# Kernel tuning notes

Measured on AMD Instinct MI355X. Metric: run time of the kernel, lower is better.

The kernel has to match this reference:

```python
import jax, jax.numpy as jnp
import numpy as np

N_NODES = 500000


def _gcn_conv(x, W, b, src, dst, n):
    # x: [N, Fin], W: [Fin, Fout]. PyG GCNConv with add_self_loops + sym norm.
    h = x @ W                                            # [N, Fout]
    deg = jax.ops.segment_sum(jnp.ones_like(dst, dtype=h.dtype), dst,
                              num_segments=n)            # in-degree incl self loops
    dinv = jnp.where(deg > 0, jax.lax.rsqrt(jnp.maximum(deg, 1)), 0.0)
    norm = dinv[src] * dinv[dst]                         # [E]
    msg = h[src] * norm[:, None]                         # gather + scale
    out = jax.ops.segment_sum(msg, dst, num_segments=n)  # scatter-add to targets
    return out + b


def setup_inputs() -> dict:
    key = jax.random.key(0)
    k1, k2, k3, k4 = jax.random.split(key, 4)
    x = jax.random.normal(k1, (N_NODES, 1), dtype=jnp.float32)
    edge_index = jax.random.randint(k2, (2, 8000000), 0, N_NODES, dtype=jnp.int64)
    W1 = jax.random.normal(k3, (1, 32), dtype=jnp.float32) * (1.0 / np.sqrt(1))
    b1 = jnp.zeros((32,), dtype=jnp.float32)
    W2 = jax.random.normal(k4, (32, 2), dtype=jnp.float32) * (1.0 / np.sqrt(32))
    b2 = jnp.zeros((2,), dtype=jnp.float32)
    return {"x": x, "edge_index": edge_index, "W1": W1, "b1": b1, "W2": W2, "b2": b2}


def reference(x, edge_index, W1, b1, W2, b2):
    n = x.shape[0]
    loops = jnp.arange(n, dtype=edge_index.dtype)
    src = jnp.concatenate([edge_index[0], loops])  # add self-loops
    dst = jnp.concatenate([edge_index[1], loops])
    h = _gcn_conv(x, W1, b1, src, dst, n)
    h = jax.nn.relu(h)
    # F.dropout(training=self.training): identity in eval mode
    h = _gcn_conv(h, W2, b2, src, dst, n)
    return jax.nn.log_softmax(h, axis=1)
```

## Files before the change

### kernel.cpp

```cpp
#include <hip/hip_runtime.h>


static constexpr int BKT_BITS = 11;
static constexpr int BKT = 1 << BKT_BITS;
static constexpr int NB = 256;
static constexpr int HB = 512;
static constexpr int HT = 256;
static constexpr int CHUNK = 8192;
static constexpr int SCT = 256;
static constexpr int PERT = CHUNK / SCT;
static constexpr int CLS_SH = 27;
static constexpr int NCLS = 8;
static constexpr int NW = 16;

using u32x4 = __attribute__((ext_vector_type(4))) unsigned;

__global__ void __launch_bounds__(HT) k_hist(const int* __restrict__ dst, int e,
                                             int chunk, int nbkt,
                                             unsigned* __restrict__ totals) {
  __shared__ unsigned cnt[NB];
  for (int t = threadIdx.x; t < NB; t += HT) cnt[t] = 0;
  __syncthreads();
  int lo = blockIdx.x * chunk;
  int hi = min(lo + chunk, e);
  const int4* d4 = (const int4*)dst;
  for (int i = (lo >> 2) + threadIdx.x; i < (hi >> 2); i += HT) {
    int4 d = d4[i];
    atomicAdd(&cnt[((unsigned)d.x) >> BKT_BITS], 1u);
    atomicAdd(&cnt[((unsigned)d.y) >> BKT_BITS], 1u);
    atomicAdd(&cnt[((unsigned)d.z) >> BKT_BITS], 1u);
    atomicAdd(&cnt[((unsigned)d.w) >> BKT_BITS], 1u);
  }
  for (int i = ((hi >> 2) << 2) + threadIdx.x; i < hi; i += HT)
    atomicAdd(&cnt[((unsigned)dst[i]) >> BKT_BITS], 1u);
  __syncthreads();
  for (int t = threadIdx.x; t < nbkt; t += HT)
    if (cnt[t]) atomicAdd(&totals[t], cnt[t]);
}

__global__ void k_basescan(const unsigned* __restrict__ totals, int nbkt,
                           unsigned* __restrict__ gcur) {
  int lane = threadIdx.x;
  unsigned running = 0;
  for (int c = 0; c < NB; c += 64) {
    int k = c + lane;
    unsigned v = (k < nbkt) ? totals[k] : 0u;
    unsigned incl = v;
#pragma unroll
    for (int off = 1; off < 64; off <<= 1) {
      unsigned t = __shfl_up(incl, off);
      if (lane >= off) incl += t;
    }
    if (k < nbkt) gcur[k] = running + incl - v;
    running += __shfl(incl, 63);
  }
}

__global__ void __launch_bounds__(SCT) k_scatter(
    const int* __restrict__ src, const int* __restrict__ dst, int e, int nbkt,
    unsigned* __restrict__ gcur, unsigned* __restrict__ packed) {
  __shared__ unsigned staged[CHUNK];
  __shared__ unsigned cnt[NB];
  __shared__ unsigned cur[NB];
  __shared__ unsigned gseg[NB];
  __shared__ unsigned loff[NB + 1];
  const int tid = threadIdx.x;
  const int lo = blockIdx.x * CHUNK;
  for (int t = tid; t < NB; t += SCT) { cnt[t] = 0u; cur[t] = 0u; }
  __syncthreads();

  unsigned pk[PERT];
  unsigned bku[PERT / 4];
  const int4* s4 = (const int4*)src;
  const int4* d4 = (const int4*)dst;
#pragma unroll
  for (int jj = 0; jj < PERT / 4; ++jj) {
    int i4 = (lo >> 2) + jj * SCT + tid;
    unsigned b4 = 0xFFFFFFFFu;
    if (i4 * 4 + 3 < e) {
      int4 s = s4[i4];
      int4 d = d4[i4];
      unsigned k0 = ((unsigned)d.x) >> BKT_BITS, k1 = ((unsigned)d.y) >> BKT_BITS;
      unsigned k2 = ((unsigned)d.z) >> BKT_BITS, k3 = ((unsigned)d.w) >> BKT_BITS;
      pk[jj * 4 + 0] = ((unsigned)s.x << BKT_BITS) | ((unsigned)d.x & (BKT - 1));
      pk[jj * 4 + 1] = ((unsigned)s.y << BKT_BITS) | ((unsigned)d.y & (BKT - 1));
      pk[jj * 4 + 2] = ((unsigned)s.z << BKT_BITS) | ((unsigned)d.z & (BKT - 1));
      pk[jj * 4 + 3] = ((unsigned)s.w << BKT_BITS) | ((unsigned)d.w & (BKT - 1));
      b4 = k0 | (k1 << 8) | (k2 << 16) | (k3 << 24);
      atomicAdd(&cnt[k0], 1u);
      atomicAdd(&cnt[k1], 1u);
      atomicAdd(&cnt[k2], 1u);
      atomicAdd(&cnt[k3], 1u);
    } else {
#pragma unroll
      for (int c = 0; c < 4; ++c) {
        int i = i4 * 4 + c;
        if (i >= lo && i < e) {
          unsigned dd = (unsigned)dst[i];
          unsigned kk = dd >> BKT_BITS;
          pk[jj * 4 + c] = ((unsigned)src[i] << BKT_BITS) | (dd & (BKT - 1));
          b4 = (b4 & ~(0xFFu << (8 * c))) | (kk << (8 * c));
          atomicAdd(&cnt[kk], 1u);
        }
      }
    }
    bku[jj] = b4;
  }
  __syncthreads();

  if (tid < 64) {
    unsigned running = 0;
    for (int c = 0; c < NB; c += 64) {
      int k = c + tid;
      unsigned v = cnt[k];
      unsigned incl = v;
#pragma unroll
      for (int off = 1; off < 64; off <<= 1) {
        unsigned t = __shfl_up(incl, off);
        if (tid >= off) incl += t;
      }
      loff[k] = running + incl - v;
      running += __shfl(incl, 63);
    }
    if (tid == 0) loff[NB] = running;
  }
  __syncthreads();

  for (int k = tid; k < nbkt; k += SCT)
    if (cnt[k]) gseg[k] = atomicAdd(&gcur[k], cnt[k]);

#pragma unroll
  for (int jj = 0; jj < PERT / 4; ++jj) {
    unsigned b4 = bku[jj];
#pragma unroll
    for (int c = 0; c < 4; ++c) {
      unsigned k = (b4 >> (8 * c)) & 0xFFu;
      if (k != 0xFFu) {
        unsigned pos = loff[k] + atomicAdd(&cur[k], 1u);
        staged[pos] = pk[jj * 4 + c];
      }
    }
  }
  __syncthreads();

  int mv = (int)loff[NB];
  for (int t = tid; t < mv; t += SCT) {
    int a = 0, b = nbkt;
    while (b - a > 1) {
      int mid = (a + b) >> 1;
      if ((int)loff[mid] <= t) a = mid; else b = mid;
    }
    __builtin_nontemporal_store(staged[t],
                                packed + gseg[a] + (unsigned)(t - (int)loff[a]));
  }
}

__global__ void __launch_bounds__(1024) k_classort(
    const unsigned* __restrict__ packed, const unsigned* __restrict__ gcur,
    const float* __restrict__ x, int n, unsigned* __restrict__ packed2,
    float* __restrict__ dinv, float* __restrict__ xs) {
  __shared__ unsigned cnt_node[BKT];
  __shared__ unsigned wcnt[NCLS * NW];
  __shared__ unsigned wcur[NCLS * NW];
  const int k = blockIdx.x;
  const int tid = threadIdx.x;
  const int w = tid >> 6;
  for (int t = tid; t < BKT; t += 1024) cnt_node[t] = 0;
  if (tid < NCLS * NW) wcnt[tid] = 0;
  __syncthreads();
  unsigned lo = k ? gcur[k - 1] : 0u, hi = gcur[k];
  unsigned loA = (lo + 3u) & ~3u, hiA = hi & ~3u;
  if (loA > hi) loA = hi;
  if (hiA < loA) hiA = loA;

  for (unsigned i = lo + tid; i < loA; i += 1024) {
    unsigned p = packed[i];
    atomicAdd(&cnt_node[p & (BKT - 1)], 1u);
    atomicAdd(&wcnt[(p >> CLS_SH) * NW + w], 1u);
  }
  for (unsigned i = hiA + tid; i < hi; i += 1024) {
    unsigned p = packed[i];
    atomicAdd(&cnt_node[p & (BKT - 1)], 1u);
    atomicAdd(&wcnt[(p >> CLS_SH) * NW + w], 1u);
  }
  const u32x4* p4 = (const u32x4*)packed;
  for (unsigned q = (loA >> 2) + tid; q < (hiA >> 2); q += 1024) {
    u32x4 p = p4[q];
    atomicAdd(&cnt_node[p.x & (BKT - 1)], 1u);
    atomicAdd(&wcnt[(p.x >> CLS_SH) * NW + w], 1u);
    atomicAdd(&cnt_node[p.y & (BKT - 1)], 1u);
    atomicAdd(&wcnt[(p.y >> CLS_SH) * NW + w], 1u);
    atomicAdd(&cnt_node[p.z & (BKT - 1)], 1u);
    atomicAdd(&wcnt[(p.z >> CLS_SH) * NW + w], 1u);
    atomicAdd(&cnt_node[p.w & (BKT - 1)], 1u);
    atomicAdd(&wcnt[(p.w >> CLS_SH) * NW + w], 1u);
  }
  __syncthreads();

  if (tid < 64) {
    unsigned running = 0;
#pragma unroll
    for (int r = 0; r < (NCLS * NW) / 64; ++r) {
      int idx = r * 64 + tid;
      unsigned v = wcnt[idx];
      unsigned incl = v;
#pragma unroll
      for (int off = 1; off < 64; off <<= 1) {
        unsigned t = __shfl_up(incl, off);
        if (tid >= off) incl += t;
      }
      wcur[idx] = running + incl - v;
      running += __shfl(incl, 63);
    }
  }
  __syncthreads();

  for (unsigned i = lo + tid; i < loA; i += 1024) {
    unsigned p = packed[i];
    unsigned pos = atomicAdd(&wcur[(p >> CLS_SH) * NW + w], 1u);
    packed2[lo + pos] = p;
  }
  for (unsigned i = hiA + tid; i < hi; i += 1024) {
    unsigned p = packed[i];
    unsigned pos = atomicAdd(&wcur[(p >> CLS_SH) * NW + w], 1u);
    packed2[lo + pos] = p;
  }
  for (unsigned q = (loA >> 2) + tid; q < (hiA >> 2); q += 1024) {
    u32x4 p = p4[q];
    unsigned pos0 = atomicAdd(&wcur[(p.x >> CLS_SH) * NW + w], 1u);
    packed2[lo + pos0] = p.x;
    unsigned pos1 = atomicAdd(&wcur[(p.y >> CLS_SH) * NW + w], 1u);
    packed2[lo + pos1] = p.y;
    unsigned pos2 = atomicAdd(&wcur[(p.z >> CLS_SH) * NW + w], 1u);
    packed2[lo + pos2] = p.z;
    unsigned pos3 = atomicAdd(&wcur[(p.w >> CLS_SH) * NW + w], 1u);
    packed2[lo + pos3] = p.w;
  }

  int g0 = k << BKT_BITS;
  for (int t = tid; t < BKT; t += 1024) {
    int g = g0 + t;
    if (g < n) {
      float di = rsqrtf((float)(cnt_node[t] + 1u));
      dinv[g] = di;
      xs[g] = di * x[g];
    }
  }
}

__global__ void __launch_bounds__(1024) k_accA2(
    const unsigned* __restrict__ packed2, const unsigned* __restrict__ gcur,
    const float* __restrict__ dinv, const float* __restrict__ xs,
    const float* __restrict__ W1, const float* __restrict__ b1,
    const float* __restrict__ W2, int n, float2* __restrict__ yd) {
  __shared__ float acc[BKT];
  __shared__ float sW1[32], sb1[32], sW2[64];
  if (threadIdx.x < 32) {
    sW1[threadIdx.x] = W1[threadIdx.x];
    sb1[threadIdx.x] = b1[threadIdx.x];
  } else if (threadIdx.x < 96) {
    sW2[threadIdx.x - 32] = W2[threadIdx.x - 32];
  }
  for (int t = threadIdx.x; t < BKT; t += 1024) acc[t] = 0.0f;
  __syncthreads();
  int k = blockIdx.x;
  unsigned lo = k ? gcur[k - 1] : 0u, hi = gcur[k];
  unsigned loA = (lo + 3u) & ~3u, hiA = hi & ~3u;
  if (loA > hi) loA = hi;
  if (hiA < loA) hiA = loA;
  for (unsigned i = lo + threadIdx.x; i < loA; i += 1024) {
    unsigned p = packed2[i];
    atomicAdd(&acc[p & (BKT - 1)], xs[p >> BKT_BITS]);
  }
  for (unsigned i = hiA + threadIdx.x; i < hi; i += 1024) {
    unsigned p = packed2[i];
    atomicAdd(&acc[p & (BKT - 1)], xs[p >> BKT_BITS]);
  }
  const u32x4* p4 = (const u32x4*)packed2;
  for (unsigned q = (loA >> 2) + threadIdx.x; q < (hiA >> 2); q += 1024) {
    u32x4 p = __builtin_nontemporal_load(p4 + q);
    float v0 = xs[p.x >> BKT_BITS];
    float v1 = xs[p.y >> BKT_BITS];
    float v2 = xs[p.z >> BKT_BITS];
    float v3 = xs[p.w >> BKT_BITS];
    atomicAdd(&acc[p.x & (BKT - 1)], v0);
    atomicAdd(&acc[p.y & (BKT - 1)], v1);
    atomicAdd(&acc[p.z & (BKT - 1)], v2);
    atomicAdd(&acc[p.w & (BKT - 1)], v3);
  }
  __syncthreads();
  int g0 = k << BKT_BITS;
  for (int t = threadIdx.x; t < BKT; t += 1024) {
    int g = g0 + t;
    if (g >= n) continue;
    float di = dinv[g];
    float s = di * (acc[t] + xs[g]);
    float y0 = 0.0f, y1 = 0.0f;
#pragma unroll
    for (int f = 0; f < 32; ++f) {
      float h = fmaxf(fmaf(s, sW1[f], sb1[f]), 0.0f);
      y0 = fmaf(h, sW2[2 * f + 0], y0);
      y1 = fmaf(h, sW2[2 * f + 1], y1);
    }
    yd[g] = make_float2(di * y0, di * y1);
  }
}

__global__ void __launch_bounds__(1024) k_accB3(
    const unsigned* __restrict__ packed2, const unsigned* __restrict__ gcur,
    const float* __restrict__ dinv, const float2* __restrict__ yd,
    const float* __restrict__ b2, int n, float2* __restrict__ out) {
  __shared__ float a0[BKT], a1[BKT];
  for (int t = threadIdx.x; t < BKT; t += 1024) {
    a0[t] = 0.0f;
    a1[t] = 0.0f;
  }
  __syncthreads();
  int k = blockIdx.x;
  unsigned lo = k ? gcur[k - 1] : 0u, hi = gcur[k];
  unsigned loA = (lo + 3u) & ~3u, hiA = hi & ~3u;
  if (loA > hi) loA = hi;
  if (hiA < loA) hiA = loA;
  for (unsigned i = lo + threadIdx.x; i < loA; i += 1024) {
    unsigned p = packed2[i];
    float2 v = yd[p >> BKT_BITS];
    atomicAdd(&a0[p & (BKT - 1)], v.x);
    atomicAdd(&a1[p & (BKT - 1)], v.y);
  }
  for (unsigned i = hiA + threadIdx.x; i < hi; i += 1024) {
    unsigned p = packed2[i];
    float2 v = yd[p >> BKT_BITS];
    atomicAdd(&a0[p & (BKT - 1)], v.x);
    atomicAdd(&a1[p & (BKT - 1)], v.y);
  }
  const u32x4* p4 = (const u32x4*)packed2;
  for (unsigned q = (loA >> 2) + threadIdx.x; q < (hiA >> 2); q += 1024) {
    u32x4 p = __builtin_nontemporal_load(p4 + q);
    float2 v0 = yd[p.x >> BKT_BITS];
    float2 v1 = yd[p.y >> BKT_BITS];
    float2 v2 = yd[p.z >> BKT_BITS];
    float2 v3 = yd[p.w >> BKT_BITS];
    atomicAdd(&a0[p.x & (BKT - 1)], v0.x);
    atomicAdd(&a1[p.x & (BKT - 1)], v0.y);
    atomicAdd(&a0[p.y & (BKT - 1)], v1.x);
    atomicAdd(&a1[p.y & (BKT - 1)], v1.y);
    atomicAdd(&a0[p.z & (BKT - 1)], v2.x);
    atomicAdd(&a1[p.z & (BKT - 1)], v2.y);
    atomicAdd(&a0[p.w & (BKT - 1)], v3.x);
    atomicAdd(&a1[p.w & (BKT - 1)], v3.y);
  }
  __syncthreads();
  float b20 = b2[0], b21 = b2[1];
  int g0 = k << BKT_BITS;
  for (int t = threadIdx.x; t < BKT; t += 1024) {
    int g = g0 + t;
    if (g >= n) continue;
    float di = dinv[g];
    float2 yv = yd[g];
    float t0 = fmaf(di, a0[t] + yv.x, b20);
    float t1 = fmaf(di, a1[t] + yv.y, b21);
    float m = fmaxf(t0, t1);
    float l = m + logf(expf(t0 - m) + expf(t1 - m));
    out[g] = make_float2(t0 - l, t1 - l);
  }
}

extern "C" void kernel_launch(void* const* d_in, const int* in_sizes, int n_in,
                              void* d_out, int out_size, void* d_ws, size_t ws_size,
                              hipStream_t stream) {
  const float* x = (const float*)d_in[0];
  const int* edge = (const int*)d_in[1];
  const float* W1 = (const float*)d_in[2];
  const float* b1 = (const float*)d_in[3];
  const float* W2 = (const float*)d_in[4];
  const float* b2 = (const float*)d_in[5];
  float2* out = (float2*)d_out;

  const int n = in_sizes[0];
  const int e = in_sizes[1] / 2;
  const int* src = edge;
  const int* dst = edge + e;

  const int nbkt = (n + BKT - 1) >> BKT_BITS;
  const int hchunk = (((e + HB - 1) / HB) + 3) & ~3;
  const int sgrid = (e + CHUNK - 1) / CHUNK;

  char* ws = (char*)d_ws;
  size_t off = 0;
  unsigned* packed = (unsigned*)(ws + off);  off += (size_t)e * 4;
  unsigned* packed2 = (unsigned*)(ws + off); off += (size_t)e * 4;
  unsigned* totals = (unsigned*)(ws + off);  off += NB * 4;
  unsigned* gcur = (unsigned*)(ws + off);    off += NB * 4;
  float* dinv = (float*)(ws + off);          off += (size_t)n * 4;
  float* xs = (float*)(ws + off);            off += (size_t)n * 4;
  float2* yd = (float2*)(ws + off);          off += (size_t)n * 8;

  hipMemsetAsync(totals, 0, NB * sizeof(unsigned), stream);
  k_hist<<<HB, HT, 0, stream>>>(dst, e, hchunk, nbkt, totals);
  k_basescan<<<1, 64, 0, stream>>>(totals, nbkt, gcur);
  k_scatter<<<sgrid, SCT, 0, stream>>>(src, dst, e, nbkt, gcur, packed);
  k_classort<<<nbkt, 1024, 0, stream>>>(packed, gcur, x, n, packed2, dinv, xs);
  k_accA2<<<nbkt, 1024, 0, stream>>>(packed2, gcur, dinv, xs, W1, b1, W2, n, yd);
  k_accB3<<<nbkt, 1024, 0, stream>>>(packed2, gcur, dinv, yd, b2, n, out);
}
```

Baseline: 253.9 us.

## Tile edge aggregation by source slice with LDS-staged features and two-way partials

```diff
diff --git a/kernel.cpp b/kernel.cpp
--- a/kernel.cpp
+++ b/kernel.cpp
@@ -9,8 +9,8 @@
 static constexpr int CHUNK = 8192;
 static constexpr int SCT = 256;
 static constexpr int PERT = CHUNK / SCT;
-static constexpr int CLS_SH = 27;
-static constexpr int NCLS = 8;
+static constexpr int NCLS = 245;
+static constexpr int NCLSP = 248;
 static constexpr int NW = 16;
 
 using u32x4 = __attribute__((ext_vector_type(4))) unsigned;
@@ -158,15 +158,16 @@
 __global__ void __launch_bounds__(1024) k_classort(
     const unsigned* __restrict__ packed, const unsigned* __restrict__ gcur,
     const float* __restrict__ x, int n, unsigned* __restrict__ packed2,
-    float* __restrict__ dinv, float* __restrict__ xs) {
+    unsigned* __restrict__ sliceoff, unsigned short* __restrict__ deg16,
+    float* __restrict__ xs) {
   __shared__ unsigned cnt_node[BKT];
-  __shared__ unsigned wcnt[NCLS * NW];
-  __shared__ unsigned wcur[NCLS * NW];
+  __shared__ unsigned wcnt[NCLSP * NW];
+  __shared__ unsigned wcur[NCLSP * NW];
   const int k = blockIdx.x;
   const int tid = threadIdx.x;
   const int w = tid >> 6;
   for (int t = tid; t < BKT; t += 1024) cnt_node[t] = 0;
-  if (tid < NCLS * NW) wcnt[tid] = 0;
+  for (int t = tid; t < NCLSP * NW; t += 1024) wcnt[t] = 0;
   __syncthreads();
   unsigned lo = k ? gcur[k - 1] : 0u, hi = gcur[k];
   unsigned loA = (lo + 3u) & ~3u, hiA = hi & ~3u;
@@ -176,32 +177,31 @@
   for (unsigned i = lo + tid; i < loA; i += 1024) {
     unsigned p = packed[i];
     atomicAdd(&cnt_node[p & (BKT - 1)], 1u);
-    atomicAdd(&wcnt[(p >> CLS_SH) * NW + w], 1u);
+    atomicAdd(&wcnt[(p >> 22) * NW + w], 1u);
   }
   for (unsigned i = hiA + tid; i < hi; i += 1024) {
     unsigned p = packed[i];
     atomicAdd(&cnt_node[p & (BKT - 1)], 1u);
-    atomicAdd(&wcnt[(p >> CLS_SH) * NW + w], 1u);
+    atomicAdd(&wcnt[(p >> 22) * NW + w], 1u);
   }
   const u32x4* p4 = (const u32x4*)packed;
   for (unsigned q = (loA >> 2) + tid; q < (hiA >> 2); q += 1024) {
     u32x4 p = p4[q];
     atomicAdd(&cnt_node[p.x & (BKT - 1)], 1u);
-    atomicAdd(&wcnt[(p.x >> CLS_SH) * NW + w], 1u);
+    atomicAdd(&wcnt[(p.x >> 22) * NW + w], 1u);
     atomicAdd(&cnt_node[p.y & (BKT - 1)], 1u);
-    atomicAdd(&wcnt[(p.y >> CLS_SH) * NW + w], 1u);
+    atomicAdd(&wcnt[(p.y >> 22) * NW + w], 1u);
     atomicAdd(&cnt_node[p.z & (BKT - 1)], 1u);
-    atomicAdd(&wcnt[(p.z >> CLS_SH) * NW + w], 1u);
+    atomicAdd(&wcnt[(p.z >> 22) * NW + w], 1u);
     atomicAdd(&cnt_node[p.w & (BKT - 1)], 1u);
-    atomicAdd(&wcnt[(p.w >> CLS_SH) * NW + w], 1u);
+    atomicAdd(&wcnt[(p.w >> 22) * NW + w], 1u);
   }
   __syncthreads();
 
   if (tid < 64) {
     unsigned running = 0;
-#pragma unroll
-    for (int r = 0; r < (NCLS * NW) / 64; ++r) {
-      int idx = r * 64 + tid;
+    for (int c = 0; c < NCLSP * NW; c += 64) {
+      int idx = c + tid;
       unsigned v = wcnt[idx];
       unsigned incl = v;
 #pragma unroll
@@ -209,7 +209,10 @@
         unsigned t = __shfl_up(incl, off);
         if (tid >= off) incl += t;
       }
-      wcur[idx] = running + incl - v;
+      unsigned excl = running + incl - v;
+      wcur[idx] = excl;
+      if ((idx & (NW - 1)) == 0 && (idx >> 4) <= NCLS)
+        sliceoff[k * (NCLS + 1) + (idx >> 4)] = excl;
       running += __shfl(incl, 63);
     }
   }
@@ -217,43 +220,73 @@
 
   for (unsigned i = lo + tid; i < loA; i += 1024) {
     unsigned p = packed[i];
-    unsigned pos = atomicAdd(&wcur[(p >> CLS_SH) * NW + w], 1u);
-    packed2[lo + pos] = p;
+    packed2[lo + atomicAdd(&wcur[(p >> 22) * NW + w], 1u)] = p;
   }
   for (unsigned i = hiA + tid; i < hi; i += 1024) {
     unsigned p = packed[i];
-    unsigned pos = atomicAdd(&wcur[(p >> CLS_SH) * NW + w], 1u);
-    packed2[lo + pos] = p;
+    packed2[lo + atomicAdd(&wcur[(p >> 22) * NW + w], 1u)] = p;
   }
   for (unsigned q = (loA >> 2) + tid; q < (hiA >> 2); q += 1024) {
     u32x4 p = p4[q];
-    unsigned pos0 = atomicAdd(&wcur[(p.x >> CLS_SH) * NW + w], 1u);
-    packed2[lo + pos0] = p.x;
-    unsigned pos1 = atomicAdd(&wcur[(p.y >> CLS_SH) * NW + w], 1u);
-    packed2[lo + pos1] = p.y;
-    unsigned pos2 = atomicAdd(&wcur[(p.z >> CLS_SH) * NW + w], 1u);
-    packed2[lo + pos2] = p.z;
-    unsigned pos3 = atomicAdd(&wcur[(p.w >> CLS_SH) * NW + w], 1u);
-    packed2[lo + pos3] = p.w;
+    packed2[lo + atomicAdd(&wcur[(p.x >> 22) * NW + w], 1u)] = p.x;
+    packed2[lo + atomicAdd(&wcur[(p.y >> 22) * NW + w], 1u)] = p.y;
+    packed2[lo + atomicAdd(&wcur[(p.z >> 22) * NW + w], 1u)] = p.z;
+    packed2[lo + atomicAdd(&wcur[(p.w >> 22) * NW + w], 1u)] = p.w;
   }
 
   int g0 = k << BKT_BITS;
   for (int t = tid; t < BKT; t += 1024) {
     int g = g0 + t;
     if (g < n) {
-      float di = rsqrtf((float)(cnt_node[t] + 1u));
-      dinv[g] = di;
-      xs[g] = di * x[g];
-    }
-  }
-}
-
-__global__ void __launch_bounds__(1024) k_accA2(
+      unsigned d = cnt_node[t];
+      deg16[g] = (unsigned short)(d > 65535u ? 65535u : d);
+      xs[g] = rsqrtf((float)(d + 1u)) * x[g];
+    }
+  }
+}
+
+__global__ void __launch_bounds__(1024) k_accA_tile(
     const unsigned* __restrict__ packed2, const unsigned* __restrict__ gcur,
-    const float* __restrict__ dinv, const float* __restrict__ xs,
-    const float* __restrict__ W1, const float* __restrict__ b1,
-    const float* __restrict__ W2, int n, float2* __restrict__ yd) {
-  __shared__ float acc[BKT];
+    const unsigned* __restrict__ sliceoff, const float* __restrict__ xs,
+    int nbkt, float* __restrict__ pA) {
+  __shared__ float acc[2 * BKT];
+  __shared__ float stg[BKT];
+  const int g = blockIdx.x >> 1, p = blockIdx.x & 1;
+  for (int t = threadIdx.x; t < 2 * BKT; t += 1024) acc[t] = 0.0f;
+  const int w = threadIdx.x >> 6, lane = threadIdx.x & 63;
+  const int bkL = w & 1, sub = w >> 1;
+  const int bk = g * 2 + bkL;
+  unsigned bs = 0, soBase = 0;
+  if (bk < nbkt) {
+    bs = bk ? gcur[bk - 1] : 0u;
+    soBase = (unsigned)bk * (NCLS + 1);
+  }
+  __syncthreads();
+  for (int s = p; s < NCLS; s += 2) {
+    for (int j = threadIdx.x; j < BKT; j += 1024)
+      stg[j] = xs[(s << BKT_BITS) + j];
+    __syncthreads();
+    if (bk < nbkt) {
+      unsigned slo = bs + sliceoff[soBase + s];
+      unsigned shi = bs + sliceoff[soBase + s + 1];
+      for (unsigned i = slo + (unsigned)(sub * 64 + lane); i < shi; i += 512u) {
+        unsigned ww = packed2[i];
+        atomicAdd(&acc[(bkL << BKT_BITS) | (ww & (BKT - 1))],
+                  stg[(ww >> BKT_BITS) & (BKT - 1)]);
+      }
+    }
+    __syncthreads();
+  }
+  float* dstp = pA + ((size_t)blockIdx.x << 12);
+  for (int t = threadIdx.x; t < 2 * BKT; t += 1024)
+    __builtin_nontemporal_store(acc[t], dstp + t);
+}
+
+__global__ void __launch_bounds__(256) k_nodeA(
+    const float* __restrict__ pA, const unsigned short* __restrict__ deg16,
+    const float* __restrict__ xs, const float* __restrict__ W1,
+    const float* __restrict__ b1, const float* __restrict__ W2, int n,
+    float2* __restrict__ yd) {
   __shared__ float sW1[32], sb1[32], sW2[64];
   if (threadIdx.x < 32) {
     sW1[threadIdx.x] = W1[threadIdx.x];
@@ -261,108 +294,82 @@
   } else if (threadIdx.x < 96) {
     sW2[threadIdx.x - 32] = W2[threadIdx.x - 32];
   }
-  for (int t = threadIdx.x; t < BKT; t += 1024) acc[t] = 0.0f;
-  __syncthreads();
-  int k = blockIdx.x;
-  unsigned lo = k ? gcur[k - 1] : 0u, hi = gcur[k];
-  unsigned loA = (lo + 3u) & ~3u, hiA = hi & ~3u;
-  if (loA > hi) loA = hi;
-  if (hiA < loA) hiA = loA;
-  for (unsigned i = lo + threadIdx.x; i < loA; i += 1024) {
-    unsigned p = packed2[i];
-    atomicAdd(&acc[p & (BKT - 1)], xs[p >> BKT_BITS]);
-  }
-  for (unsigned i = hiA + threadIdx.x; i < hi; i += 1024) {
-    unsigned p = packed2[i];
-    atomicAdd(&acc[p & (BKT - 1)], xs[p >> BKT_BITS]);
-  }
-  const u32x4* p4 = (const u32x4*)packed2;
-  for (unsigned q = (loA >> 2) + threadIdx.x; q < (hiA >> 2); q += 1024) {
-    u32x4 p = __builtin_nontemporal_load(p4 + q);
-    float v0 = xs[p.x >> BKT_BITS];
-    float v1 = xs[p.y >> BKT_BITS];
-    float v2 = xs[p.z >> BKT_BITS];
-    float v3 = xs[p.w >> BKT_BITS];
-    atomicAdd(&acc[p.x & (BKT - 1)], v0);
-    atomicAdd(&acc[p.y & (BKT - 1)], v1);
-    atomicAdd(&acc[p.z & (BKT - 1)], v2);
-    atomicAdd(&acc[p.w & (BKT - 1)], v3);
-  }
-  __syncthreads();
-  int g0 = k << BKT_BITS;
-  for (int t = threadIdx.x; t < BKT; t += 1024) {
-    int g = g0 + t;
-    if (g >= n) continue;
-    float di = dinv[g];
-    float s = di * (acc[t] + xs[g]);
-    float y0 = 0.0f, y1 = 0.0f;
-#pragma unroll
-    for (int f = 0; f < 32; ++f) {
-      float h = fmaxf(fmaf(s, sW1[f], sb1[f]), 0.0f);
-      y0 = fmaf(h, sW2[2 * f + 0], y0);
-      y1 = fmaf(h, sW2[2 * f + 1], y1);
-    }
-    yd[g] = make_float2(di * y0, di * y1);
-  }
-}
-
-__global__ void __launch_bounds__(1024) k_accB3(
+  __syncthreads();
+  int g = blockIdx.x * 256 + threadIdx.x;
+  if (g >= n) return;
+  int gr = g >> 12, local = g & 4095;
+  float a = pA[((size_t)(gr * 2) << 12) + local] +
+            pA[((size_t)(gr * 2 + 1) << 12) + local];
+  float di = rsqrtf((float)(deg16[g] + 1u));
+  float sv = di * (a + xs[g]);
+  float y0 = 0.0f, y1 = 0.0f;
+#pragma unroll
+  for (int f = 0; f < 32; ++f) {
+    float h = fmaxf(fmaf(sv, sW1[f], sb1[f]), 0.0f);
+    y0 = fmaf(h, sW2[2 * f + 0], y0);
+    y1 = fmaf(h, sW2[2 * f + 1], y1);
+  }
+  yd[g] = make_float2(di * y0, di * y1);
+}
+
+__global__ void __launch_bounds__(1024) k_accB_tile(
     const unsigned* __restrict__ packed2, const unsigned* __restrict__ gcur,
-    const float* __restrict__ dinv, const float2* __restrict__ yd,
-    const float* __restrict__ b2, int n, float2* __restrict__ out) {
-  __shared__ float a0[BKT], a1[BKT];
-  for (int t = threadIdx.x; t < BKT; t += 1024) {
+    const unsigned* __restrict__ sliceoff, const float2* __restrict__ yd,
+    int nbkt, float2* __restrict__ pB) {
+  __shared__ float a0[2 * BKT], a1[2 * BKT];
+  __shared__ float2 stg[BKT];
+  const int g = blockIdx.x >> 1, p = blockIdx.x & 1;
+  for (int t = threadIdx.x; t < 2 * BKT; t += 1024) {
     a0[t] = 0.0f;
     a1[t] = 0.0f;
   }
-  __syncthreads();
-  int k = blockIdx.x;
-  unsigned lo = k ? gcur[k - 1] : 0u, hi = gcur[k];
-  unsigned loA = (lo + 3u) & ~3u, hiA = hi & ~3u;
-  if (loA > hi) loA = hi;
-  if (hiA < loA) hiA = loA;
-  for (unsigned i = lo + threadIdx.x; i < loA; i += 1024) {
-    unsigned p = packed2[i];
-    float2 v = yd[p >> BKT_BITS];
-    atomicAdd(&a0[p & (BKT - 1)], v.x);
-    atomicAdd(&a1[p & (BKT - 1)], v.y);
-  }
-  for (unsigned i = hiA + threadIdx.x; i < hi; i += 1024) {
-    unsigned p = packed2[i];
-    float2 v = yd[p >> BKT_BITS];
-    atomicAdd(&a0[p & (BKT - 1)], v.x);
-    atomicAdd(&a1[p & (BKT - 1)], v.y);
-  }
-  const u32x4* p4 = (const u32x4*)packed2;
-  for (unsigned q = (loA >> 2) + threadIdx.x; q < (hiA >> 2); q += 1024) {
-    u32x4 p = __builtin_nontemporal_load(p4 + q);
-    float2 v0 = yd[p.x >> BKT_BITS];
-    float2 v1 = yd[p.y >> BKT_BITS];
-    float2 v2 = yd[p.z >> BKT_BITS];
-    float2 v3 = yd[p.w >> BKT_BITS];
-    atomicAdd(&a0[p.x & (BKT - 1)], v0.x);
-    atomicAdd(&a1[p.x & (BKT - 1)], v0.y);
-    atomicAdd(&a0[p.y & (BKT - 1)], v1.x);
-    atomicAdd(&a1[p.y & (BKT - 1)], v1.y);
-    atomicAdd(&a0[p.z & (BKT - 1)], v2.x);
-    atomicAdd(&a1[p.z & (BKT - 1)], v2.y);
-    atomicAdd(&a0[p.w & (BKT - 1)], v3.x);
-    atomicAdd(&a1[p.w & (BKT - 1)], v3.y);
-  }
-  __syncthreads();
-  float b20 = b2[0], b21 = b2[1];
-  int g0 = k << BKT_BITS;
-  for (int t = threadIdx.x; t < BKT; t += 1024) {
-    int g = g0 + t;
-    if (g >= n) continue;
-    float di = dinv[g];
-    float2 yv = yd[g];
-    float t0 = fmaf(di, a0[t] + yv.x, b20);
-    float t1 = fmaf(di, a1[t] + yv.y, b21);
-    float m = fmaxf(t0, t1);
-    float l = m + logf(expf(t0 - m) + expf(t1 - m));
-    out[g] = make_float2(t0 - l, t1 - l);
-  }
+  const int w = threadIdx.x >> 6, lane = threadIdx.x & 63;
+  const int bkL = w & 1, sub = w >> 1;
+  const int bk = g * 2 + bkL;
+  unsigned bs = 0, soBase = 0;
+  if (bk < nbkt) {
+    bs = bk ? gcur[bk - 1] : 0u;
+    soBase = (unsigned)bk * (NCLS + 1);
+  }
+  __syncthreads();
+  for (int s = p; s < NCLS; s += 2) {
+    for (int j = threadIdx.x; j < BKT; j += 1024)
+      stg[j] = yd[(s << BKT_BITS) + j];
+    __syncthreads();
+    if (bk < nbkt) {
+      unsigned slo = bs + sliceoff[soBase + s];
+      unsigned shi = bs + sliceoff[soBase + s + 1];
+      for (unsigned i = slo + (unsigned)(sub * 64 + lane); i < shi; i += 512u) {
+        unsigned ww = packed2[i];
+        unsigned d = (bkL << BKT_BITS) | (ww & (BKT - 1));
+        float2 v = stg[(ww >> BKT_BITS) & (BKT - 1)];
+        atomicAdd(&a0[d], v.x);
+        atomicAdd(&a1[d], v.y);
+      }
+    }
+    __syncthreads();
+  }
+  float2* dstp = pB + ((size_t)blockIdx.x << 12);
+  for (int t = threadIdx.x; t < 2 * BKT; t += 1024)
+    dstp[t] = make_float2(a0[t], a1[t]);
+}
+
+__global__ void __launch_bounds__(256) k_nodeB(
+    const float2* __restrict__ pB, const unsigned short* __restrict__ deg16,
+    const float2* __restrict__ yd, const float* __restrict__ b2, int n,
+    float2* __restrict__ out) {
+  int g = blockIdx.x * 256 + threadIdx.x;
+  if (g >= n) return;
+  int gr = g >> 12, local = g & 4095;
+  float2 v0 = pB[((size_t)(gr * 2) << 12) + local];
+  float2 v1 = pB[((size_t)(gr * 2 + 1) << 12) + local];
+  float di = rsqrtf((float)(deg16[g] + 1u));
+  float2 yv = yd[g];
+  float t0 = fmaf(di, v0.x + v1.x + yv.x, b2[0]);
+  float t1 = fmaf(di, v0.y + v1.y + yv.y, b2[1]);
+  float m = fmaxf(t0, t1);
+  float l = m + logf(expf(t0 - m) + expf(t1 - m));
+  out[g] = make_float2(t0 - l, t1 - l);
 }
 
 extern "C" void kernel_launch(void* const* d_in, const int* in_sizes, int n_in,
@@ -384,22 +391,32 @@
   const int nbkt = (n + BKT - 1) >> BKT_BITS;
   const int hchunk = (((e + HB - 1) / HB) + 3) & ~3;
   const int sgrid = (e + CHUNK - 1) / CHUNK;
+  const int ngrid = (n + 255) / 256;
+  const int ngrp2 = (nbkt + 1) / 2;
 
   char* ws = (char*)d_ws;
   size_t off = 0;
-  unsigned* packed = (unsigned*)(ws + off);  off += (size_t)e * 4;
-  unsigned* packed2 = (unsigned*)(ws + off); off += (size_t)e * 4;
-  unsigned* totals = (unsigned*)(ws + off);  off += NB * 4;
-  unsigned* gcur = (unsigned*)(ws + off);    off += NB * 4;
-  float* dinv = (float*)(ws + off);          off += (size_t)n * 4;
-  float* xs = (float*)(ws + off);            off += (size_t)n * 4;
-  float2* yd = (float2*)(ws + off);          off += (size_t)n * 8;
+  unsigned* packed = (unsigned*)(ws + off);   off += (size_t)e * 4;
+  unsigned* packed2 = (unsigned*)(ws + off);  off += (size_t)e * 4;
+  unsigned* totals = (unsigned*)(ws + off);   off += NB * 4;
+  unsigned* gcur = (unsigned*)(ws + off);     off += NB * 4;
+  unsigned* sliceoff = (unsigned*)(ws + off); off += (size_t)nbkt * (NCLS + 1) * 4;
+  unsigned short* deg16 = (unsigned short*)(ws + off); off += (size_t)n * 2;
+  float* xs = (float*)(ws + off);             off += (size_t)n * 4;
+  float2* yd = (float2*)(ws + off);           off += (size_t)n * 8;
+  float* pA = (float*)packed;
+  float2* pB = (float2*)(ws + (size_t)8 * 1024 * 1024);
 
   hipMemsetAsync(totals, 0, NB * sizeof(unsigned), stream);
   k_hist<<<HB, HT, 0, stream>>>(dst, e, hchunk, nbkt, totals);
   k_basescan<<<1, 64, 0, stream>>>(totals, nbkt, gcur);
   k_scatter<<<sgrid, SCT, 0, stream>>>(src, dst, e, nbkt, gcur, packed);
-  k_classort<<<nbkt, 1024, 0, stream>>>(packed, gcur, x, n, packed2, dinv, xs);
-  k_accA2<<<nbkt, 1024, 0, stream>>>(packed2, gcur, dinv, xs, W1, b1, W2, n, yd);
-  k_accB3<<<nbkt, 1024, 0, stream>>>(packed2, gcur, dinv, yd, b2, n, out);
-}
+  k_classort<<<nbkt, 1024, 0, stream>>>(packed, gcur, x, n, packed2, sliceoff,
+                                        deg16, xs);
+  k_accA_tile<<<ngrp2 * 2, 1024, 0, stream>>>(packed2, gcur, sliceoff, xs, nbkt,
+                                              pA);
+  k_nodeA<<<ngrid, 256, 0, stream>>>(pA, deg16, xs, W1, b1, W2, n, yd);
+  k_accB_tile<<<ngrp2 * 2, 1024, 0, stream>>>(packed2, gcur, sliceoff, yd, nbkt,
+                                              pB);
+  k_nodeB<<<ngrid, 256, 0, stream>>>(pB, deg16, yd, b2, n, out);
+}
```

Result: slower. 543.9 us (+114.2%).
